# Optimization experiments

Hardware: AMD Instinct MI355X
Metric: run time of the kernel (lower is better)

## Reference

```python
import jax, jax.numpy as jnp
import numpy as np

C_S = 384
C_Z = 128
C_OUT = 1


def setup_inputs() -> dict:
    key = jax.random.key(0)
    k1, k2, k3 = jax.random.split(key, 3)
    B, N = 1, 1024
    s = jax.random.normal(k1, (B, N, C_S), dtype=jnp.float32)
    z = jax.random.normal(k2, (B, N, N, C_Z), dtype=jnp.float32)
    # Linear(2*c_s + c_z -> c_out); init='final' zeros weights in the original,
    # use small random weights for a meaningful correctness baseline.
    W = jax.random.normal(k3, (C_OUT, 2 * C_S + C_Z), dtype=jnp.float32) * 0.02
    b = jnp.zeros((C_OUT,), dtype=jnp.float32)
    return {"s": s, "z": z, "W": W, "b": b}


def reference(s, z, W, b):
    # Mathematically identical to cat([s_i, s_j, z], -1) @ W.T + b, but
    # decomposed so the (B,N,N,2*c_s+c_z) intermediate is never materialized.
    Wi = W[:, :C_S]            # weights hitting s_i (broadcast over j)
    Wj = W[:, C_S:2 * C_S]     # weights hitting s_j (broadcast over i)
    Wz = W[:, 2 * C_S:]        # weights hitting z
    si = jnp.einsum('bnd,od->bno', s, Wi)          # [B,N,c_out]
    sj = jnp.einsum('bnd,od->bno', s, Wj)          # [B,N,c_out]
    zz = jnp.einsum('bnmc,oc->bnmo', z, Wz)        # [B,N,N,c_out]
    logits = si[:, :, None, :] + sj[:, None, :, :] + zz + b
    return logits
```

## Files before the change

### kernel.cpp

```cpp
#include <hip/hip_runtime.h>

#define C_S 384
#define C_Z 128
#define N_SEQ 1024

__global__ __launch_bounds__(256) void sisj_kernel(const float* __restrict__ s,
                                                   const float* __restrict__ W,
                                                   const float* __restrict__ b,
                                                   float* __restrict__ si,
                                                   float* __restrict__ sj) {
    const int lane = threadIdx.x & 63;
    const int wave = threadIdx.x >> 6;
    const int n = blockIdx.x * 4 + wave;

    const float* srow = s + (size_t)n * C_S;
    const float* Wi = W;
    const float* Wj = W + C_S;

    float acc_i = 0.f, acc_j = 0.f;
#pragma unroll
    for (int j = 0; j < C_S / 64; ++j) {
        const int idx = lane + 64 * j;
        const float v = srow[idx];
        acc_i += v * Wi[idx];
        acc_j += v * Wj[idx];
    }
#pragma unroll
    for (int mask = 32; mask >= 1; mask >>= 1) {
        acc_i += __shfl_xor(acc_i, mask);
        acc_j += __shfl_xor(acc_j, mask);
    }
    if (lane == 0) {
        si[n] = acc_i;
        sj[n] = acc_j + b[0];
    }
}

__global__ __launch_bounds__(256) void contact_kernel(const float* __restrict__ z,
                                                      const float* __restrict__ W,
                                                      const float* __restrict__ si,
                                                      const float* __restrict__ sj,
                                                      float* __restrict__ out) {
    const int lane = threadIdx.x & 63;
    const int wave = threadIdx.x >> 6;
    const int half = lane >> 5;
    const int l = lane & 31;
    const long long gw = (long long)blockIdx.x * 4 + wave;
    const long long o = gw * 2 + half;

    const float4 wz = *(const float4*)(W + 2 * C_S + 4 * l);

    const float4 z4 = *(const float4*)(z + (o << 7) + 4 * l);

    float p = z4.x * wz.x + z4.y * wz.y + z4.z * wz.z + z4.w * wz.w;

#pragma unroll
    for (int mask = 16; mask >= 1; mask >>= 1) {
        p += __shfl_xor(p, mask);
    }

    if (l == 0) {
        const int n = (int)(o >> 10);
        const int m = (int)(o & 1023);
        out[o] = p + si[n] + sj[m];
    }
}

extern "C" void kernel_launch(void* const* d_in, const int* in_sizes, int n_in,
                              void* d_out, int out_size, void* d_ws, size_t ws_size,
                              hipStream_t stream) {
    const float* s = (const float*)d_in[0];
    const float* z = (const float*)d_in[1];
    const float* W = (const float*)d_in[2];
    const float* b = (const float*)d_in[3];
    float* out = (float*)d_out;

    float* si = (float*)d_ws;
    float* sj = si + N_SEQ;

    sisj_kernel<<<N_SEQ / 4, 256, 0, stream>>>(s, W, b, si, sj);

    const int total_outputs = N_SEQ * N_SEQ;
    const int blocks = total_outputs / (2 * 4);
    contact_kernel<<<blocks, 256, 0, stream>>>(z, W, si, sj, out);
}
```

Baseline: 673.8 us.

## Compute one output per thread with serial float4 dot product over z row

Replaces the half-wave-per-output layout and its shuffle reduction with one thread per output that loops over the 128-channel z row in float4 chunks. It removes the cross-lane reduction, the idle lanes at store time and the very large grid. In exchange, adjacent threads now read addresses 512 bytes apart, so each load is uncoalesced and relies on cache reuse across loop iterations.

Measured after the change: 687.4 us. 2.0% more time.

```diff
diff --git a/kernel.cpp b/kernel.cpp
--- a/kernel.cpp
+++ b/kernel.cpp
@@ -41,29 +41,22 @@
                                                       const float* __restrict__ si,
                                                       const float* __restrict__ sj,
                                                       float* __restrict__ out) {
-    const int lane = threadIdx.x & 63;
-    const int wave = threadIdx.x >> 6;
-    const int half = lane >> 5;
-    const int l = lane & 31;
-    const long long gw = (long long)blockIdx.x * 4 + wave;
-    const long long o = gw * 2 + half;
+    const int o = blockIdx.x * 256 + threadIdx.x;
+    const float4* __restrict__ zr = (const float4*)(z + ((size_t)o << 7));
+    const float4* __restrict__ wz = (const float4*)(W + 2 * C_S);
 
-    const float4 wz = *(const float4*)(W + 2 * C_S + 4 * l);
-
-    const float4 z4 = *(const float4*)(z + (o << 7) + 4 * l);
-
-    float p = z4.x * wz.x + z4.y * wz.y + z4.z * wz.z + z4.w * wz.w;
-
-#pragma unroll
-    for (int mask = 16; mask >= 1; mask >>= 1) {
-        p += __shfl_xor(p, mask);
+    float4 acc = make_float4(0.f, 0.f, 0.f, 0.f);
+#pragma unroll 8
+    for (int k = 0; k < C_Z / 4; ++k) {
+        const float4 a = zr[k];
+        const float4 w = wz[k];
+        acc.x += a.x * w.x;
+        acc.y += a.y * w.y;
+        acc.z += a.z * w.z;
+        acc.w += a.w * w.w;
     }
-
-    if (l == 0) {
-        const int n = (int)(o >> 10);
-        const int m = (int)(o & 1023);
-        out[o] = p + si[n] + sj[m];
-    }
+    const float p = (acc.x + acc.y) + (acc.z + acc.w);
+    out[o] = p + si[o >> 10] + sj[o & 1023];
 }
 
 extern "C" void kernel_launch(void* const* d_in, const int* in_sizes, int n_in,
@@ -80,7 +73,5 @@
 
     sisj_kernel<<<N_SEQ / 4, 256, 0, stream>>>(s, W, b, si, sj);
 
-    const int total_outputs = N_SEQ * N_SEQ;
-    const int blocks = total_outputs / (2 * 4);
-    contact_kernel<<<blocks, 256, 0, stream>>>(z, W, si, sj, out);
+    contact_kernel<<<(N_SEQ * N_SEQ) / 256, 256, 0, stream>>>(z, W, si, sj, out);
 }
```
